# Kernel tuning notes

Measured on AMD Instinct MI355X. Metric: run time of the kernel, lower is better.

Reference implementation:

```python
import jax, jax.numpy as jnp
import numpy as np

E, N, D, DFF, NE = 8, 4096, 1024, 2048, 65536

def setup_inputs() -> dict:
    key = jax.random.key(0)
    k1, k2, k3, k4 = jax.random.split(key, 4)
    x = jax.random.normal(k1, (E, N, D), dtype=jnp.float32)
    W1 = jax.random.normal(k2, (E, D, DFF), dtype=jnp.float32) * (1.0 / np.sqrt(D))
    W2 = jax.random.normal(k3, (E, DFF, D), dtype=jnp.float32) * (1.0 / np.sqrt(DFF))
    edge_index = jax.random.randint(k4, (2, NE), 0, N, dtype=jnp.int64)
    return {"x": x, "W1": W1, "W2": W2, "edge_index": edge_index}

def reference(x, W1, W2, edge_index):
    # Vectorized form of the per-expert Python loop + stack:
    # each expert: h = relu(x_e @ W1_e); agg[dst] += h[src]; out_e = agg @ W2_e
    n = x.shape[1]
    src, dst = edge_index[0], edge_index[1]
    h = jax.nn.relu(jnp.einsum('end,edf->enf', x, W1))  # [e, n, dff]
    msgs = h[:, src, :]                                  # [e, n_edges, dff] (irregular gather)
    agg = jax.vmap(lambda m: jax.ops.segment_sum(m, dst, num_segments=n))(msgs)  # [e, n, dff]
    out = jnp.einsum('enf,efd->end', agg, W2)            # [e, n, d] == x.shape
    return out
```

## Files before the change

### kernel.cpp

```cpp
#include <hip/hip_runtime.h>

#define E_ 8
#define N_ 4096
#define D_ 1024
#define DFF_ 2048
#define NE_ 65536

typedef __attribute__((ext_vector_type(8))) short short8;
typedef __attribute__((ext_vector_type(4))) float f32x4;

__device__ __forceinline__ unsigned short f2bf(float f) {
  unsigned u = __float_as_uint(f);
  u += 0x7fffu + ((u >> 16) & 1u);
  return (unsigned short)(u >> 16);
}
__device__ __forceinline__ float bf2f(unsigned short h) {
  return __uint_as_float(((unsigned)h) << 16);
}


__global__ __launch_bounds__(256) void cvt_f32_bf16_vec(
    const float* __restrict__ in, unsigned short* __restrict__ out, int n4) {
  int i = blockIdx.x * 256 + threadIdx.x;
  if (i >= n4) return;
  float4 v = ((const float4*)in)[i];
  ushort4 o;
  o.x = f2bf(v.x); o.y = f2bf(v.y); o.z = f2bf(v.z); o.w = f2bf(v.w);
  ((ushort4*)out)[i] = o;
}

__global__ __launch_bounds__(256) void transpose_cvt(
    const float* __restrict__ in, unsigned short* __restrict__ out, int R, int C) {
  __shared__ float tile[32][33];
  const int e = blockIdx.z;
  const float* ine = in + (size_t)e * R * C;
  unsigned short* oute = out + (size_t)e * R * C;
  const int c0 = blockIdx.x * 32, r0 = blockIdx.y * 32;
  const int tx = threadIdx.x & 31, ty = threadIdx.x >> 5;
#pragma unroll
  for (int i = 0; i < 32; i += 8)
    tile[ty + i][tx] = ine[(size_t)(r0 + ty + i) * C + (c0 + tx)];
  __syncthreads();
#pragma unroll
  for (int i = 0; i < 32; i += 8)
    oute[(size_t)(c0 + ty + i) * R + (r0 + tx)] = f2bf(tile[tx][ty + i]);
}


__global__ __launch_bounds__(256) void zero_i32(int* __restrict__ p, int n) {
  int i = blockIdx.x * 256 + threadIdx.x;
  if (i < n) p[i] = 0;
}

__global__ __launch_bounds__(256) void hist_dst(
    const int* __restrict__ ei, int* __restrict__ cnt, int ne) {
  int i = blockIdx.x * 256 + threadIdx.x;
  if (i < ne) atomicAdd(&cnt[ei[ne + i]], 1);
}

__global__ __launch_bounds__(1024) void scan4096(
    const int* __restrict__ cnt, int* __restrict__ rowptr, int* __restrict__ cursor) {
  __shared__ int tmp[1024];
  const int tid = threadIdx.x;
  const int b = tid * 4;
  int c0 = cnt[b + 0], c1 = cnt[b + 1], c2 = cnt[b + 2], c3 = cnt[b + 3];
  int tot = c0 + c1 + c2 + c3;
  tmp[tid] = tot;
  __syncthreads();
  int val = tot;
  for (int off = 1; off < 1024; off <<= 1) {
    int v = 0;
    if (tid >= off) v = tmp[tid - off];
    __syncthreads();
    val += v;
    tmp[tid] = val;
    __syncthreads();
  }
  const int excl = val - tot;
  rowptr[b + 0] = excl;
  rowptr[b + 1] = excl + c0;
  rowptr[b + 2] = excl + c0 + c1;
  rowptr[b + 3] = excl + c0 + c1 + c2;
  cursor[b + 0] = excl;
  cursor[b + 1] = excl + c0;
  cursor[b + 2] = excl + c0 + c1;
  cursor[b + 3] = excl + c0 + c1 + c2;
  if (tid == 1023) rowptr[N_] = val;
}

__global__ __launch_bounds__(256) void fill_csr(
    const int* __restrict__ ei, int* __restrict__ cursor, int* __restrict__ csr, int ne) {
  int i = blockIdx.x * 256 + threadIdx.x;
  if (i < ne) {
    int s = ei[i];
    int d = ei[ne + i];
    int pos = atomicAdd(&cursor[d], 1);
    csr[pos] = s;
  }
}


#define BAR() asm volatile("s_barrier" ::: "memory")
#define WAIT_VM(n) asm volatile("s_waitcnt vmcnt(" #n ")" ::: "memory")

template <bool RELU>
__global__ __launch_bounds__(512, 1) void gemm256(
    const unsigned short* __restrict__ A, const unsigned short* __restrict__ BT,
    unsigned short* __restrict__ Cb, int M, int Nm, int K, int nbx, int nbxy) {
  __shared__ char lds[131072];

  const int orig = blockIdx.x;
  const int sw = (orig & 7) * nbxy + (orig >> 3);
  const int e = sw / nbxy;
  const int rem = sw - e * nbxy;
  const int by = rem / nbx;
  const int bx = rem - by * nbx;
  const int m0 = by * 256, n0 = bx * 256;

  const int tid = threadIdx.x;
  const int lane = tid & 63;
  const int wid = tid >> 6;
  const int wm = wid >> 2;
  const int wn = wid & 3;
  const int lo = lane & 15, hi = lane >> 4;

  const unsigned short* Ae = A + (size_t)e * M * K + (size_t)m0 * K;
  const unsigned short* Be = BT + (size_t)e * Nm * K + (size_t)n0 * K;
  unsigned short* Ce = Cb + (size_t)e * M * Nm;

  auto srcoff = [&](int p) -> size_t {
    int R = p >> 3, s = p & 7;
    int bc = s ^ (R & 7);
    int gr = 2 * R + (bc >> 2), c = bc & 3;
    return (size_t)gr * K + (size_t)c * 8;
  };
  const size_t so0 = srcoff(tid);
  const size_t so1 = srcoff(tid + 512);

#define GLD(src_, dst_)                                                        \
  __builtin_amdgcn_global_load_lds(                                            \
      (const __attribute__((address_space(1))) void*)(src_),                   \
      (__attribute__((address_space(3))) void*)(dst_), 16, 0, 0)

#define STAGE(t_)                                                              \
  do {                                                                         \
    char* Lb_ = lds + ((t_) & 3) * 32768;                                      \
    const unsigned short* ga_ = Ae + (size_t)(t_) * 32;                        \
    const unsigned short* gb_ = Be + (size_t)(t_) * 32;                        \
    GLD(ga_ + so0, Lb_ + tid * 16);                                            \
    GLD(ga_ + so1, Lb_ + 8192 + tid * 16);                                     \
    GLD(gb_ + so0, Lb_ + 16384 + tid * 16);                                    \
    GLD(gb_ + so1, Lb_ + 24576 + tid * 16);                                    \
  } while (0)

  const int slot = (((lo & 1) << 2) | hi) ^ ((lo >> 1) & 7);
  const int aoff = (wm * 64 + (lo >> 1)) * 128 + slot * 16;
  const int boff = 16384 + (wn * 32 + (lo >> 1)) * 128 + slot * 16;

  f32x4 acc[8][4];
#pragma unroll
  for (int i = 0; i < 8; ++i)
#pragma unroll
    for (int j = 0; j < 4; ++j) acc[i][j] = (f32x4){0.f, 0.f, 0.f, 0.f};

  auto tile_body = [&](int t, bool dostage) {
    const char* L = lds + (t & 3) * 32768;
    short8 af[8], bfv[4];
#pragma unroll
    for (int fm = 0; fm < 8; ++fm) af[fm] = *(const short8*)(L + aoff + fm * 1024);
#pragma unroll
    for (int fn = 0; fn < 4; ++fn) bfv[fn] = *(const short8*)(L + boff + fn * 1024);
    if (dostage) STAGE(t + 3);
#pragma unroll
    for (int fm = 0; fm < 8; ++fm)
#pragma unroll
      for (int fn = 0; fn < 4; ++fn)
        acc[fm][fn] = __builtin_amdgcn_mfma_f32_16x16x32_bf16(af[fm], bfv[fn],
                                                              acc[fm][fn], 0, 0, 0);
  };

  const int nkt = K >> 5;

  STAGE(0);
  STAGE(1);
  STAGE(2);

  int t = 0;
  for (; t < nkt - 3; ++t) {
    WAIT_VM(8);
    BAR();
    tile_body(t, true);
  }
  WAIT_VM(8); BAR(); tile_body(nkt - 3, false);
  WAIT_VM(4); BAR(); tile_body(nkt - 2, false);
  WAIT_VM(0); BAR(); tile_body(nkt - 1, false);

  const int row0 = m0 + wm * 128 + hi * 4;
  const int col0 = n0 + wn * 64 + lo;
#pragma unroll
  for (int fm = 0; fm < 8; ++fm)
#pragma unroll
    for (int fn = 0; fn < 4; ++fn)
#pragma unroll
      for (int r = 0; r < 4; ++r) {
        float v = acc[fm][fn][r];
        if (RELU) v = fmaxf(v, 0.f);
        Ce[(size_t)(row0 + fm * 16 + r) * Nm + (col0 + fn * 16)] = f2bf(v);
      }
#undef STAGE
#undef GLD
}


__global__ __launch_bounds__(256) void gather_sum(
    const unsigned short* __restrict__ y, const int* __restrict__ rowptr,
    const int* __restrict__ csr, float* __restrict__ out) {
  const int dst = blockIdx.x;
  const int e = blockIdx.y;
  const unsigned short* ye = y + (size_t)e * N_ * D_;
  float* oute = out + (size_t)e * N_ * D_ + (size_t)dst * D_;
  const int t = threadIdx.x;
  const int beg = rowptr[dst], end = rowptr[dst + 1];
  float a0 = 0.f, a1 = 0.f, a2 = 0.f, a3 = 0.f;
  for (int i = beg; i < end; ++i) {
    const int s = csr[i];
    ushort4 v = ((const ushort4*)(ye + (size_t)s * D_))[t];
    a0 += bf2f(v.x);
    a1 += bf2f(v.y);
    a2 += bf2f(v.z);
    a3 += bf2f(v.w);
  }
  float4 o;
  o.x = a0; o.y = a1; o.z = a2; o.w = a3;
  ((float4*)oute)[t] = o;
}


extern "C" void kernel_launch(void* const* d_in, const int* in_sizes, int n_in,
                              void* d_out, int out_size, void* d_ws, size_t ws_size,
                              hipStream_t stream) {
  (void)in_sizes; (void)n_in; (void)out_size; (void)ws_size;
  const float* x = (const float*)d_in[0];
  const float* W1 = (const float*)d_in[1];
  const float* W2 = (const float*)d_in[2];
  const int* ei = (const int*)d_in[3];
  float* out = (float*)d_out;

  char* p = (char*)d_ws;
  auto alloc = [&](size_t b) {
    char* r = p;
    p += (b + 255) & ~(size_t)255;
    return r;
  };
  unsigned short* xbf = (unsigned short*)alloc((size_t)E_ * N_ * D_ * 2);
  unsigned short* w1t = (unsigned short*)alloc((size_t)E_ * D_ * DFF_ * 2);
  unsigned short* w2t = (unsigned short*)alloc((size_t)E_ * DFF_ * D_ * 2);
  unsigned short* h = (unsigned short*)alloc((size_t)E_ * N_ * DFF_ * 2);
  unsigned short* y = (unsigned short*)alloc((size_t)E_ * N_ * D_ * 2);
  int* cnt = (int*)alloc((size_t)N_ * 4);
  int* rowptr = (int*)alloc((size_t)(N_ + 1) * 4);
  int* cursor = (int*)alloc((size_t)N_ * 4);
  int* csr = (int*)alloc((size_t)NE_ * 4);

  cvt_f32_bf16_vec<<<(E_ * N_ * D_ / 4 + 255) / 256, 256, 0, stream>>>(x, xbf, E_ * N_ * D_ / 4);
  transpose_cvt<<<dim3(DFF_ / 32, D_ / 32, E_), 256, 0, stream>>>(W1, w1t, D_, DFF_);
  transpose_cvt<<<dim3(D_ / 32, DFF_ / 32, E_), 256, 0, stream>>>(W2, w2t, DFF_, D_);

  zero_i32<<<(N_ + 255) / 256, 256, 0, stream>>>(cnt, N_);
  hist_dst<<<NE_ / 256, 256, 0, stream>>>(ei, cnt, NE_);
  scan4096<<<1, 1024, 0, stream>>>(cnt, rowptr, cursor);
  fill_csr<<<NE_ / 256, 256, 0, stream>>>(ei, cursor, csr, NE_);

  {
    int nbx = DFF_ / 256, nby = N_ / 256;
    gemm256<true><<<nbx * nby * E_, 512, 0, stream>>>(xbf, w1t, h, N_, DFF_, D_, nbx, nbx * nby);
  }
  {
    int nbx = D_ / 256, nby = N_ / 256;
    gemm256<false><<<nbx * nby * E_, 512, 0, stream>>>(h, w2t, y, N_, D_, DFF_, nbx, nbx * nby);
  }

  gather_sum<<<dim3(N_, E_), 256, 0, stream>>>(y, rowptr, csr, out);
}
```

Baseline: 500.5 us.

## Double-buffer LDS fragment reads in registers to overlap with MFMA

The GEMM main loop now unrolls by two and keeps two register sets of A/B fragments. Each tile's LDS reads are issued before the MFMAs of the previous tile run, so LDS latency can hide behind matrix math. The MFMA blocks are also wrapped in s_setprio to favour the math wave. The cost is roughly double the fragment registers, which may lower occupancy or cause spills, and the loop now assumes an even tile count.

```diff
diff --git a/kernel.cpp b/kernel.cpp
--- a/kernel.cpp
+++ b/kernel.cpp
@@ -163,20 +163,24 @@
 #pragma unroll
     for (int j = 0; j < 4; ++j) acc[i][j] = (f32x4){0.f, 0.f, 0.f, 0.f};
 
-  auto tile_body = [&](int t, bool dostage) {
+  short8 afA[8], bfA[4], afB[8], bfB[4];
+
+  auto dsread = [&](short8* af, short8* bfv, int t) {
     const char* L = lds + (t & 3) * 32768;
-    short8 af[8], bfv[4];
 #pragma unroll
     for (int fm = 0; fm < 8; ++fm) af[fm] = *(const short8*)(L + aoff + fm * 1024);
 #pragma unroll
     for (int fn = 0; fn < 4; ++fn) bfv[fn] = *(const short8*)(L + boff + fn * 1024);
-    if (dostage) STAGE(t + 3);
+  };
+  auto domfma = [&](const short8* af, const short8* bfv) {
+    __builtin_amdgcn_s_setprio(1);
 #pragma unroll
     for (int fm = 0; fm < 8; ++fm)
 #pragma unroll
       for (int fn = 0; fn < 4; ++fn)
         acc[fm][fn] = __builtin_amdgcn_mfma_f32_16x16x32_bf16(af[fm], bfv[fn],
                                                               acc[fm][fn], 0, 0, 0);
+    __builtin_amdgcn_s_setprio(0);
   };
 
   const int nkt = K >> 5;
@@ -184,16 +188,29 @@
   STAGE(0);
   STAGE(1);
   STAGE(2);
+  WAIT_VM(8);
+  BAR();
+  dsread(afA, bfA, 0);
 
   int t = 0;
-  for (; t < nkt - 3; ++t) {
-    WAIT_VM(8);
+  for (; t + 1 < nkt - 2; t += 2) {
+    WAIT_VM(4);
     BAR();
-    tile_body(t, true);
-  }
-  WAIT_VM(8); BAR(); tile_body(nkt - 3, false);
-  WAIT_VM(4); BAR(); tile_body(nkt - 2, false);
-  WAIT_VM(0); BAR(); tile_body(nkt - 1, false);
+    dsread(afB, bfB, t + 1);
+    if (t + 3 < nkt) STAGE(t + 3);
+    domfma(afA, bfA);
+
+    WAIT_VM(4);
+    BAR();
+    dsread(afA, bfA, t + 2);
+    if (t + 4 < nkt) STAGE(t + 4);
+    domfma(afB, bfB);
+  }
+  WAIT_VM(0);
+  BAR();
+  dsread(afB, bfB, nkt - 1);
+  domfma(afA, bfA);
+  domfma(afB, bfB);
 
   const int row0 = m0 + wm * 128 + hi * 4;
   const int col0 = n0 + wn * 64 + lo;
```

After: 493.3 us. No clear change (-1.4%).

## Restructure GEMM main loop into 8-wave ping-pong schedule with half-tile staging

Applied to the files above, without the earlier changes.

The GEMM main loop now works on K-tiles of 64 split into halves, with two 64KB LDS buffers. Each tile runs as four phases that interleave LDS fragment reads, asynchronous global-to-LDS loads for future tiles, and MFMA bursts wrapped in s_setprio, so loads and math overlap more finely. The gather kernel gets an XCD-aware block swizzle over a flattened grid and a two-way unrolled edge loop to put more loads in flight. The trade-off is more barriers per tile and a more fragile hand-scheduled wait-count sequence.

```diff
diff --git a/kernel.cpp b/kernel.cpp
--- a/kernel.cpp
+++ b/kernel.cpp
@@ -101,6 +101,7 @@
 
 
 #define BAR() asm volatile("s_barrier" ::: "memory")
+#define LGKM0() asm volatile("s_waitcnt lgkmcnt(0)" ::: "memory")
 #define WAIT_VM(n) asm volatile("s_waitcnt vmcnt(" #n ")" ::: "memory")
 
 template <bool RELU>
@@ -142,20 +143,16 @@
       (const __attribute__((address_space(1))) void*)(src_),                   \
       (__attribute__((address_space(3))) void*)(dst_), 16, 0, 0)
 
-#define STAGE(t_)                                                              \
+#define STAGE_HALF(gsrc_, b_, h_)                                              \
   do {                                                                         \
-    char* Lb_ = lds + ((t_) & 3) * 32768;                                      \
-    const unsigned short* ga_ = Ae + (size_t)(t_) * 32;                        \
-    const unsigned short* gb_ = Be + (size_t)(t_) * 32;                        \
-    GLD(ga_ + so0, Lb_ + tid * 16);                                            \
-    GLD(ga_ + so1, Lb_ + 8192 + tid * 16);                                     \
-    GLD(gb_ + so0, Lb_ + 16384 + tid * 16);                                    \
-    GLD(gb_ + so1, Lb_ + 24576 + tid * 16);                                    \
+    char* Lb_ = lds + (b_) * 65536 + (h_) * 16384;                             \
+    GLD((gsrc_) + so0, Lb_ + tid * 16);                                        \
+    GLD((gsrc_) + so1, Lb_ + 8192 + tid * 16);                                 \
   } while (0)
 
   const int slot = (((lo & 1) << 2) | hi) ^ ((lo >> 1) & 7);
-  const int aoff = (wm * 64 + (lo >> 1)) * 128 + slot * 16;
-  const int boff = 16384 + (wn * 32 + (lo >> 1)) * 128 + slot * 16;
+  const int aoff = wm * 8192 + (lo >> 1) * 128 + slot * 16;
+  const int boff = wn * 4096 + (lo >> 1) * 128 + slot * 16;
 
   f32x4 acc[8][4];
 #pragma unroll
@@ -163,37 +160,80 @@
 #pragma unroll
     for (int j = 0; j < 4; ++j) acc[i][j] = (f32x4){0.f, 0.f, 0.f, 0.f};
 
-  auto tile_body = [&](int t, bool dostage) {
-    const char* L = lds + (t & 3) * 32768;
-    short8 af[8], bfv[4];
-#pragma unroll
-    for (int fm = 0; fm < 8; ++fm) af[fm] = *(const short8*)(L + aoff + fm * 1024);
-#pragma unroll
-    for (int fn = 0; fn < 4; ++fn) bfv[fn] = *(const short8*)(L + boff + fn * 1024);
-    if (dostage) STAGE(t + 3);
+  short8 af[8], bfv[2];
+
+  auto readA = [&](const char* LA) {
+#pragma unroll
+    for (int fm = 0; fm < 8; ++fm) af[fm] = *(const short8*)(LA + aoff + fm * 1024);
+  };
+  auto readB2 = [&](const char* LB, int f0) {
+#pragma unroll
+    for (int j = 0; j < 2; ++j) bfv[j] = *(const short8*)(LB + boff + (f0 + j) * 1024);
+  };
+  auto mfma16 = [&](int FN0) {
+    __builtin_amdgcn_s_setprio(1);
 #pragma unroll
     for (int fm = 0; fm < 8; ++fm)
 #pragma unroll
-      for (int fn = 0; fn < 4; ++fn)
-        acc[fm][fn] = __builtin_amdgcn_mfma_f32_16x16x32_bf16(af[fm], bfv[fn],
-                                                              acc[fm][fn], 0, 0, 0);
-  };
-
-  const int nkt = K >> 5;
-
-  STAGE(0);
-  STAGE(1);
-  STAGE(2);
-
-  int t = 0;
-  for (; t < nkt - 3; ++t) {
-    WAIT_VM(8);
+      for (int j = 0; j < 2; ++j)
+        acc[fm][FN0 + j] = __builtin_amdgcn_mfma_f32_16x16x32_bf16(
+            af[fm], bfv[j], acc[fm][FN0 + j], 0, 0, 0);
+    __builtin_amdgcn_s_setprio(0);
+  };
+
+  const int nkt = K >> 6;
+
+  STAGE_HALF(Ae, 0, 0);
+  STAGE_HALF(Ae + 32, 0, 1);
+  STAGE_HALF(Be, 0, 2);
+  STAGE_HALF(Be + 32, 0, 3);
+  STAGE_HALF(Ae + 64, 1, 0);
+  STAGE_HALF(Be + 64, 1, 2);
+  STAGE_HALF(Ae + 96, 1, 1);
+  WAIT_VM(6);
+  BAR();
+
+  for (int t = 0; t < nkt; ++t) {
+    const int buf = t & 1;
+    const char* L = lds + buf * 65536;
+    const char* LA0 = L;
+    const char* LA1 = L + 16384;
+    const char* LB0 = L + 32768;
+    const char* LB1 = L + 49152;
+    const size_t g1 = (size_t)(t + 1) * 64;
+    const size_t g2 = (size_t)(t + 2) * 64;
+
+    readA(LA0);
+    readB2(LB0, 0);
+    if (t + 1 < nkt) STAGE_HALF(Be + g1 + 32, buf ^ 1, 3);
+    BAR(); LGKM0();
+    mfma16(0);
     BAR();
-    tile_body(t, true);
-  }
-  WAIT_VM(8); BAR(); tile_body(nkt - 3, false);
-  WAIT_VM(4); BAR(); tile_body(nkt - 2, false);
-  WAIT_VM(0); BAR(); tile_body(nkt - 1, false);
+
+    readB2(LB0, 2);
+    if (t + 2 < nkt) STAGE_HALF(Ae + g2, buf, 0);
+    BAR(); LGKM0();
+    mfma16(2);
+    BAR();
+
+    readA(LA1);
+    readB2(LB1, 0);
+    if (t + 2 < nkt) STAGE_HALF(Be + g2, buf, 2);
+    BAR(); LGKM0();
+    mfma16(0);
+    BAR();
+
+    readB2(LB1, 2);
+    if (t + 2 < nkt) STAGE_HALF(Ae + g2 + 32, buf, 1);
+    BAR(); LGKM0();
+    mfma16(2);
+    if (t + 2 < nkt) {
+      WAIT_VM(6);
+    } else {
+      WAIT_VM(0);
+    }
+    BAR();
+  }
 
   const int row0 = m0 + wm * 128 + hi * 4;
   const int col0 = n0 + wn * 64 + lo;
@@ -207,7 +247,7 @@
         if (RELU) v = fmaxf(v, 0.f);
         Ce[(size_t)(row0 + fm * 16 + r) * Nm + (col0 + fn * 16)] = f2bf(v);
       }
-#undef STAGE
+#undef STAGE_HALF
 #undef GLD
 }
 
@@ -215,20 +255,29 @@
 __global__ __launch_bounds__(256) void gather_sum(
     const unsigned short* __restrict__ y, const int* __restrict__ rowptr,
     const int* __restrict__ csr, float* __restrict__ out) {
-  const int dst = blockIdx.x;
-  const int e = blockIdx.y;
+  const int orig = blockIdx.x;
+  const int sw = (orig & 7) * (E_ * N_ / 8) + (orig >> 3);
+  const int e = sw >> 12;
+  const int dst = sw & 4095;
   const unsigned short* ye = y + (size_t)e * N_ * D_;
   float* oute = out + (size_t)e * N_ * D_ + (size_t)dst * D_;
   const int t = threadIdx.x;
   const int beg = rowptr[dst], end = rowptr[dst + 1];
   float a0 = 0.f, a1 = 0.f, a2 = 0.f, a3 = 0.f;
-  for (int i = beg; i < end; ++i) {
+  int i = beg;
+  for (; i + 1 < end; i += 2) {
+    const int s0 = csr[i], s1 = csr[i + 1];
+    ushort4 v0 = ((const ushort4*)(ye + (size_t)s0 * D_))[t];
+    ushort4 v1 = ((const ushort4*)(ye + (size_t)s1 * D_))[t];
+    a0 += bf2f(v0.x) + bf2f(v1.x);
+    a1 += bf2f(v0.y) + bf2f(v1.y);
+    a2 += bf2f(v0.z) + bf2f(v1.z);
+    a3 += bf2f(v0.w) + bf2f(v1.w);
+  }
+  if (i < end) {
     const int s = csr[i];
     ushort4 v = ((const ushort4*)(ye + (size_t)s * D_))[t];
-    a0 += bf2f(v.x);
-    a1 += bf2f(v.y);
-    a2 += bf2f(v.z);
-    a3 += bf2f(v.w);
+    a0 += bf2f(v.x); a1 += bf2f(v.y); a2 += bf2f(v.z); a3 += bf2f(v.w);
   }
   float4 o;
   o.x = a0; o.y = a1; o.z = a2; o.w = a3;
@@ -280,5 +329,5 @@
     gemm256<false><<<nbx * nby * E_, 512, 0, stream>>>(h, w2t, y, N_, D_, DFF_, nbx, nbx * nby);
   }
 
-  gather_sum<<<dim3(N_, E_), 256, 0, stream>>>(y, rowptr, csr, out);
-}
+  gather_sum<<<E_ * N_, 256, 0, stream>>>(y, rowptr, csr, out);
+}
```

New measurement: 473.9 us. -5.3%, faster.

## Shrink GEMM tiles to 128x128 with 3-stage buffering and swizzle gather blocks

Applied to the files above, without the earlier changes.

Replaces the 256x256, 512-thread GEMM that held one block per CU with a 128x128, 256-thread GEMM. It uses 48KB of LDS in a 3-buffer ring, so up to 3 blocks can share a CU and hide latency. The gather-sum kernel now uses a flat grid with an expert-interleaving swizzle and processes two edges per iteration to raise memory-level parallelism. Smaller tiles reuse less data per block and raise global and L2 traffic, and the prefetch depth drops from 3 tiles to 2.

```diff
diff --git a/kernel.cpp b/kernel.cpp
--- a/kernel.cpp
+++ b/kernel.cpp
@@ -104,10 +104,10 @@
 #define WAIT_VM(n) asm volatile("s_waitcnt vmcnt(" #n ")" ::: "memory")
 
 template <bool RELU>
-__global__ __launch_bounds__(512, 1) void gemm256(
+__global__ __launch_bounds__(256, 3) void gemm128(
     const unsigned short* __restrict__ A, const unsigned short* __restrict__ BT,
     unsigned short* __restrict__ Cb, int M, int Nm, int K, int nbx, int nbxy) {
-  __shared__ char lds[131072];
+  __shared__ char lds[49152];
 
   const int orig = blockIdx.x;
   const int sw = (orig & 7) * nbxy + (orig >> 3);
@@ -115,13 +115,13 @@
   const int rem = sw - e * nbxy;
   const int by = rem / nbx;
   const int bx = rem - by * nbx;
-  const int m0 = by * 256, n0 = bx * 256;
+  const int m0 = by * 128, n0 = bx * 128;
 
   const int tid = threadIdx.x;
   const int lane = tid & 63;
   const int wid = tid >> 6;
-  const int wm = wid >> 2;
-  const int wn = wid & 3;
+  const int wm = wid >> 1;
+  const int wn = wid & 1;
   const int lo = lane & 15, hi = lane >> 4;
 
   const unsigned short* Ae = A + (size_t)e * M * K + (size_t)m0 * K;
@@ -135,70 +135,73 @@
     return (size_t)gr * K + (size_t)c * 8;
   };
   const size_t so0 = srcoff(tid);
-  const size_t so1 = srcoff(tid + 512);
+  const size_t so1 = srcoff(tid + 256);
 
 #define GLD(src_, dst_)                                                        \
   __builtin_amdgcn_global_load_lds(                                            \
       (const __attribute__((address_space(1))) void*)(src_),                   \
       (__attribute__((address_space(3))) void*)(dst_), 16, 0, 0)
 
-#define STAGE(t_)                                                              \
+#define STAGE(t_, bs_)                                                         \
   do {                                                                         \
-    char* Lb_ = lds + ((t_) & 3) * 32768;                                      \
+    char* Lb_ = lds + (bs_) * 16384;                                           \
     const unsigned short* ga_ = Ae + (size_t)(t_) * 32;                        \
     const unsigned short* gb_ = Be + (size_t)(t_) * 32;                        \
     GLD(ga_ + so0, Lb_ + tid * 16);                                            \
-    GLD(ga_ + so1, Lb_ + 8192 + tid * 16);                                     \
-    GLD(gb_ + so0, Lb_ + 16384 + tid * 16);                                    \
-    GLD(gb_ + so1, Lb_ + 24576 + tid * 16);                                    \
+    GLD(ga_ + so1, Lb_ + 4096 + tid * 16);                                     \
+    GLD(gb_ + so0, Lb_ + 8192 + tid * 16);                                     \
+    GLD(gb_ + so1, Lb_ + 12288 + tid * 16);                                    \
   } while (0)
 
   const int slot = (((lo & 1) << 2) | hi) ^ ((lo >> 1) & 7);
-  const int aoff = (wm * 64 + (lo >> 1)) * 128 + slot * 16;
-  const int boff = 16384 + (wn * 32 + (lo >> 1)) * 128 + slot * 16;
-
-  f32x4 acc[8][4];
-#pragma unroll
-  for (int i = 0; i < 8; ++i)
+  const int aoff = wm * 4096 + (lo >> 1) * 128 + slot * 16;
+  const int boff = 8192 + wn * 4096 + (lo >> 1) * 128 + slot * 16;
+
+  f32x4 acc[4][4];
+#pragma unroll
+  for (int i = 0; i < 4; ++i)
 #pragma unroll
     for (int j = 0; j < 4; ++j) acc[i][j] = (f32x4){0.f, 0.f, 0.f, 0.f};
 
-  auto tile_body = [&](int t, bool dostage) {
-    const char* L = lds + (t & 3) * 32768;
-    short8 af[8], bfv[4];
-#pragma unroll
-    for (int fm = 0; fm < 8; ++fm) af[fm] = *(const short8*)(L + aoff + fm * 1024);
+  const int nkt = K >> 5;
+
+  STAGE(0, 0);
+  STAGE(1, 1);
+
+  int bc = 0;
+  for (int t = 0; t < nkt; ++t) {
+    if (t < nkt - 1) {
+      WAIT_VM(4);
+    } else {
+      WAIT_VM(0);
+    }
+    BAR();
+
+    const char* L = lds + bc * 16384;
+    short8 af[4], bfv[4];
+#pragma unroll
+    for (int fm = 0; fm < 4; ++fm) af[fm] = *(const short8*)(L + aoff + fm * 1024);
 #pragma unroll
     for (int fn = 0; fn < 4; ++fn) bfv[fn] = *(const short8*)(L + boff + fn * 1024);
-    if (dostage) STAGE(t + 3);
-#pragma unroll
-    for (int fm = 0; fm < 8; ++fm)
+
+    if (t + 2 < nkt) {
+      const int bs = bc == 0 ? 2 : bc - 1;
+      STAGE(t + 2, bs);
+    }
+
+#pragma unroll
+    for (int fm = 0; fm < 4; ++fm)
 #pragma unroll
       for (int fn = 0; fn < 4; ++fn)
         acc[fm][fn] = __builtin_amdgcn_mfma_f32_16x16x32_bf16(af[fm], bfv[fn],
                                                               acc[fm][fn], 0, 0, 0);
-  };
-
-  const int nkt = K >> 5;
-
-  STAGE(0);
-  STAGE(1);
-  STAGE(2);
-
-  int t = 0;
-  for (; t < nkt - 3; ++t) {
-    WAIT_VM(8);
-    BAR();
-    tile_body(t, true);
-  }
-  WAIT_VM(8); BAR(); tile_body(nkt - 3, false);
-  WAIT_VM(4); BAR(); tile_body(nkt - 2, false);
-  WAIT_VM(0); BAR(); tile_body(nkt - 1, false);
-
-  const int row0 = m0 + wm * 128 + hi * 4;
+    bc = bc == 2 ? 0 : bc + 1;
+  }
+
+  const int row0 = m0 + wm * 64 + hi * 4;
   const int col0 = n0 + wn * 64 + lo;
 #pragma unroll
-  for (int fm = 0; fm < 8; ++fm)
+  for (int fm = 0; fm < 4; ++fm)
 #pragma unroll
     for (int fn = 0; fn < 4; ++fn)
 #pragma unroll
@@ -215,20 +218,29 @@
 __global__ __launch_bounds__(256) void gather_sum(
     const unsigned short* __restrict__ y, const int* __restrict__ rowptr,
     const int* __restrict__ csr, float* __restrict__ out) {
-  const int dst = blockIdx.x;
-  const int e = blockIdx.y;
+  const int orig = blockIdx.x;
+  const int sw = (orig & 7) * (E_ * N_ / 8) + (orig >> 3);
+  const int e = sw >> 12;
+  const int dst = sw & 4095;
   const unsigned short* ye = y + (size_t)e * N_ * D_;
   float* oute = out + (size_t)e * N_ * D_ + (size_t)dst * D_;
   const int t = threadIdx.x;
   const int beg = rowptr[dst], end = rowptr[dst + 1];
   float a0 = 0.f, a1 = 0.f, a2 = 0.f, a3 = 0.f;
-  for (int i = beg; i < end; ++i) {
+  int i = beg;
+  for (; i + 1 < end; i += 2) {
+    const int s0 = csr[i], s1 = csr[i + 1];
+    ushort4 v0 = ((const ushort4*)(ye + (size_t)s0 * D_))[t];
+    ushort4 v1 = ((const ushort4*)(ye + (size_t)s1 * D_))[t];
+    a0 += bf2f(v0.x) + bf2f(v1.x);
+    a1 += bf2f(v0.y) + bf2f(v1.y);
+    a2 += bf2f(v0.z) + bf2f(v1.z);
+    a3 += bf2f(v0.w) + bf2f(v1.w);
+  }
+  if (i < end) {
     const int s = csr[i];
     ushort4 v = ((const ushort4*)(ye + (size_t)s * D_))[t];
-    a0 += bf2f(v.x);
-    a1 += bf2f(v.y);
-    a2 += bf2f(v.z);
-    a3 += bf2f(v.w);
+    a0 += bf2f(v.x); a1 += bf2f(v.y); a2 += bf2f(v.z); a3 += bf2f(v.w);
   }
   float4 o;
   o.x = a0; o.y = a1; o.z = a2; o.w = a3;
@@ -272,13 +284,13 @@
   fill_csr<<<NE_ / 256, 256, 0, stream>>>(ei, cursor, csr, NE_);
 
   {
-    int nbx = DFF_ / 256, nby = N_ / 256;
-    gemm256<true><<<nbx * nby * E_, 512, 0, stream>>>(xbf, w1t, h, N_, DFF_, D_, nbx, nbx * nby);
+    int nbx = DFF_ / 128, nby = N_ / 128;
+    gemm128<true><<<nbx * nby * E_, 256, 0, stream>>>(xbf, w1t, h, N_, DFF_, D_, nbx, nbx * nby);
   }
   {
-    int nbx = D_ / 256, nby = N_ / 256;
-    gemm256<false><<<nbx * nby * E_, 512, 0, stream>>>(h, w2t, y, N_, D_, DFF_, nbx, nbx * nby);
-  }
-
-  gather_sum<<<dim3(N_, E_), 256, 0, stream>>>(y, rowptr, csr, out);
-}
+    int nbx = D_ / 128, nby = N_ / 128;
+    gemm128<false><<<nbx * nby * E_, 256, 0, stream>>>(h, w2t, y, N_, D_, DFF_, nbx, nbx * nby);
+  }
+
+  gather_sum<<<E_ * N_, 256, 0, stream>>>(y, rowptr, csr, out);
+}
```

Measured after the change: 529.9 us. 1.06x slower.
